# Optimization experiments

Hardware: AMD Instinct MI355X
Metric: run time of the kernel (lower is better)

The kernel has to match this reference:

```python
import jax, jax.numpy as jnp
import numpy as np

N_HEADS = 32
N_KV_HEADS = 8


def _rope_tables(T, half_dim):
    # standard rotary angle tables: theta_i = 10000^(-2i/D)
    inv_freq = 1.0 / (10000.0 ** (np.arange(half_dim, dtype=np.float32) / half_dim))
    ang = np.arange(T, dtype=np.float32)[:, None] * inv_freq[None, :]  # [T, D/2]
    return jnp.asarray(np.sin(ang)), jnp.asarray(np.cos(ang))


def setup_inputs() -> dict:
    key = jax.random.key(0)
    ks = jax.random.split(key, 5)
    B, T, C = 1, 2048, 2048
    hd = C // N_HEADS  # 64
    kv_dim = N_KV_HEADS * hd  # 512
    w_scale = 0.02
    x = jax.random.normal(ks[0], (B, T, C), dtype=jnp.float32)
    Wq = jax.random.normal(ks[1], (C, C), dtype=jnp.float32) * w_scale
    Wk = jax.random.normal(ks[2], (C, kv_dim), dtype=jnp.float32) * w_scale
    Wv = jax.random.normal(ks[3], (C, kv_dim), dtype=jnp.float32) * w_scale
    Wo = jax.random.normal(ks[4], (C, C), dtype=jnp.float32) * w_scale
    rope_sin, rope_cos = _rope_tables(T, hd // 2)
    return {"x": x, "Wq": Wq, "Wk": Wk, "Wv": Wv, "Wo": Wo,
            "rope_sin": rope_sin, "rope_cos": rope_cos, "swa_window": 1024}


def apply_rope(x, sin, cos):
    # x: [B, T, H, D]; sin/cos: [T, D/2]; interleaved-pair rotation
    B, T, H, D = x.shape
    xr = x.reshape(B, T, H, D // 2, 2)
    x1, x2 = xr[..., 0], xr[..., 1]
    s = sin[None, :, None, :]
    c = cos[None, :, None, :]
    o1 = x1 * c - x2 * s
    o2 = x1 * s + x2 * c
    return jnp.stack((o1, o2), axis=-1).reshape(B, T, H, D)


def reference(x, Wq, Wk, Wv, Wo, rope_sin, rope_cos, swa_window):
    B, T, C = x.shape
    hd = C // N_HEADS
    g = N_HEADS // N_KV_HEADS
    q = (x @ Wq).reshape(B, T, N_HEADS, hd)
    k = (x @ Wk).reshape(B, T, N_KV_HEADS, hd)
    v = (x @ Wv).reshape(B, T, N_KV_HEADS, hd)
    q = apply_rope(q, rope_sin, rope_cos)
    k = apply_rope(k, rope_sin, rope_cos)
    # GQA: expand kv heads (repeat_interleave along head dim)
    k = jnp.repeat(k, g, axis=2)
    v = jnp.repeat(v, g, axis=2)
    q = q.transpose(0, 2, 1, 3)  # [B, H, T, D]
    k = k.transpose(0, 2, 1, 3)
    v = v.transpose(0, 2, 1, 3)
    scores = jnp.einsum('bhqd,bhkd->bhqk', q, k) / jnp.sqrt(jnp.float32(hd))
    idx = jnp.arange(T)
    rel = idx[:, None] - idx[None, :]  # query_pos - key_pos
    # masked-out: future tokens (rel < 0) or older than the sliding window
    masked = (rel < 0) | (rel > swa_window)
    scores = jnp.where(masked[None, None], jnp.float32(-1e30), scores)
    attn = jax.nn.softmax(scores, axis=-1)
    out = jnp.einsum('bhqk,bhkd->bhqd', attn, v)
    out = out.transpose(0, 2, 1, 3).reshape(B, T, C)
    return out @ Wo
```

## Files before the change

kernel.cpp:

```cpp
#include <hip/hip_runtime.h>

typedef __attribute__((ext_vector_type(8))) short short8;
typedef __attribute__((ext_vector_type(4))) float f32x4;
typedef unsigned short u16;

#define T_SEQ 2048
#define C_DIM 2048
#define QKV_N 3072
#define HD 64


static __device__ __forceinline__ u16 f2bf(float f) {
    unsigned u = __builtin_bit_cast(unsigned, f);
    unsigned rounding = 0x7fffu + ((u >> 16) & 1u);
    return (u16)((u + rounding) >> 16);
}

static __device__ __forceinline__ void gld_lds16(void* lds, const void* g) {
    __builtin_amdgcn_global_load_lds(
        (const __attribute__((address_space(1))) unsigned int*)g,
        (__attribute__((address_space(3))) unsigned int*)lds, 16, 0, 0);
}


__global__ __launch_bounds__(256) void convert_bf16_k(const float* __restrict__ in,
                                                      u16* __restrict__ out) {
    int i = (blockIdx.x * 256 + threadIdx.x) * 4;
    f32x4 v = *(const f32x4*)(in + i);
    u16* o = out + i;
    o[0] = f2bf(v[0]); o[1] = f2bf(v[1]); o[2] = f2bf(v[2]); o[3] = f2bf(v[3]);
}


__global__ __launch_bounds__(256) void transpose_all(const float* __restrict__ Wq,
                                                     const float* __restrict__ Wk,
                                                     const float* __restrict__ Wv,
                                                     const float* __restrict__ Wo,
                                                     u16* __restrict__ Wt,
                                                     u16* __restrict__ Wot) {
    __shared__ float tile[32][33];
    int bx = blockIdx.x;
    const float* W; u16* D; int N, row_off;
    if (bx < 64)      { W = Wq; D = Wt;  N = 2048; row_off = 0;    }
    else if (bx < 80) { W = Wk; D = Wt;  N = 512;  row_off = 2048; bx -= 64; }
    else if (bx < 96) { W = Wv; D = Wt;  N = 512;  row_off = 2560; bx -= 80; }
    else              { W = Wo; D = Wot; N = 2048; row_off = 0;    bx -= 96; }
    int n0 = bx * 32, k0 = blockIdx.y * 32;
    int tx = threadIdx.x & 31, ty = threadIdx.x >> 5;
#pragma unroll
    for (int i = 0; i < 4; i++)
        tile[ty + i * 8][tx] = W[(size_t)(k0 + ty + i * 8) * N + n0 + tx];
    __syncthreads();
#pragma unroll
    for (int i = 0; i < 4; i++)
        D[(size_t)(row_off + n0 + ty + i * 8) * 2048 + k0 + tx] = f2bf(tile[tx][ty + i * 8]);
}


__global__ __launch_bounds__(256) void gemm_bt(const u16* __restrict__ A,
                                               const u16* __restrict__ BT,
                                               float* __restrict__ C,
                                               int M, int N, int K) {
    __shared__ alignas(16) u16 As[2][128][64];
    __shared__ alignas(16) u16 Bs[2][128][64];
    const int m0 = blockIdx.x * 128;
    const int n0 = blockIdx.y * 128;
    const int w = threadIdx.x >> 6, lane = threadIdx.x & 63;
    const int lo = lane & 15, hi = lane >> 4;
    const int wr = w >> 1, wc = w & 1;
    const int srcsw = ((lane & 7) ^ (lane >> 3)) * 8;

    f32x4 zero4 = {0.f, 0.f, 0.f, 0.f};
    f32x4 acc[4][4];
#pragma unroll
    for (int m = 0; m < 4; m++)
#pragma unroll
        for (int n = 0; n < 4; n++) acc[m][n] = zero4;

    auto stage = [&](int buf, int k0) {
#pragma unroll
        for (int j = 0; j < 4; j++) {
            int row = (w * 4 + j) * 8 + (lane >> 3);
            gld_lds16((char*)&As[buf][0][0] + (w * 4 + j) * 1024,
                      A + (size_t)(m0 + row) * K + k0 + srcsw);
            gld_lds16((char*)&Bs[buf][0][0] + (w * 4 + j) * 1024,
                      BT + (size_t)(n0 + row) * K + k0 + srcsw);
        }
    };

    stage(0, 0);
    __syncthreads();
    const int nk = K >> 6;
    for (int t = 0; t < nk; t++) {
        const int cur = t & 1;
        if (t + 1 < nk) stage(cur ^ 1, (t + 1) * 64);
#pragma unroll
        for (int kk = 0; kk < 2; kk++) {
            short8 a[4], b[4];
#pragma unroll
            for (int m = 0; m < 4; m++) {
                int r = wr * 64 + m * 16 + lo;
                a[m] = *(const short8*)((const char*)&As[cur][0][0] + r * 128 + (((kk * 4 + hi) ^ (lo & 7)) << 4));
            }
#pragma unroll
            for (int n = 0; n < 4; n++) {
                int r = wc * 64 + n * 16 + lo;
                b[n] = *(const short8*)((const char*)&Bs[cur][0][0] + r * 128 + (((kk * 4 + hi) ^ (lo & 7)) << 4));
            }
#pragma unroll
            for (int m = 0; m < 4; m++)
#pragma unroll
                for (int n = 0; n < 4; n++)
                    acc[m][n] = __builtin_amdgcn_mfma_f32_16x16x32_bf16(a[m], b[n], acc[m][n], 0, 0, 0);
        }
        __syncthreads();
    }
#pragma unroll
    for (int m = 0; m < 4; m++)
#pragma unroll
        for (int n = 0; n < 4; n++) {
            int col = n0 + wc * 64 + n * 16 + lo;
#pragma unroll
            for (int r = 0; r < 4; r++) {
                int row = m0 + wr * 64 + m * 16 + hi * 4 + r;
                C[(size_t)row * N + col] = acc[m][n][r];
            }
        }
}


__global__ __launch_bounds__(256) void rope_conv(const float* __restrict__ qkv,
                                                 const float* __restrict__ sn,
                                                 const float* __restrict__ cs,
                                                 u16* __restrict__ qb,
                                                 u16* __restrict__ kb,
                                                 u16* __restrict__ vt) {
    int t = blockIdx.x / 6;
    int idx = (blockIdx.x % 6) * 256 + threadIdx.x;
    const float* row = qkv + (size_t)t * QKV_N;
    if (idx < 1024) {
        int h = idx >> 5, pr = idx & 31;
        float x1 = row[h * 64 + 2 * pr], x2 = row[h * 64 + 2 * pr + 1];
        float s = sn[t * 32 + pr], c = cs[t * 32 + pr];
        float o1 = (x1 * c - x2 * s) * 0.125f;
        float o2 = (x1 * s + x2 * c) * 0.125f;
        unsigned pack = (unsigned)f2bf(o1) | ((unsigned)f2bf(o2) << 16);
        *(unsigned*)(qb + (size_t)t * C_DIM + h * 64 + 2 * pr) = pack;
    } else if (idx < 1280) {
        int j = idx - 1024;
        int kh = j >> 5, pr = j & 31;
        float x1 = row[2048 + kh * 64 + 2 * pr], x2 = row[2048 + kh * 64 + 2 * pr + 1];
        float s = sn[t * 32 + pr], c = cs[t * 32 + pr];
        float o1 = x1 * c - x2 * s;
        float o2 = x1 * s + x2 * c;
        unsigned pack = (unsigned)f2bf(o1) | ((unsigned)f2bf(o2) << 16);
        *(unsigned*)(kb + ((size_t)kh * T_SEQ + t) * 64 + 2 * pr) = pack;
    } else {
        int j = idx - 1280;
        int kh = j >> 5, dl = (j & 31) * 2;
        float v0 = row[2560 + kh * 64 + dl], v1 = row[2560 + kh * 64 + dl + 1];
        vt[((size_t)kh * 64 + dl) * T_SEQ + t] = f2bf(v0);
        vt[((size_t)kh * 64 + dl + 1) * T_SEQ + t] = f2bf(v1);
    }
}


__global__ __launch_bounds__(256) void attn_fwd(const u16* __restrict__ qb,
                                                const u16* __restrict__ kb,
                                                const u16* __restrict__ vt,
                                                u16* __restrict__ ob,
                                                const int* __restrict__ winp) {
    __shared__ alignas(16) char KsB[2][8192];
    __shared__ alignas(16) char VsB[2][8192];
    __shared__ alignas(16) u16 Ps[4][16][88];
    const int window = *winp;
    const int h = blockIdx.y, kvh = h >> 2;
    const int q0 = blockIdx.x * 64;
    const int w = threadIdx.x >> 6, lane = threadIdx.x & 63;
    const int lo = lane & 15, hi = lane >> 4;

    const int qrow = q0 + w * 16 + lo;
    const short8 qa0 = *(const short8*)(qb + (size_t)qrow * C_DIM + h * HD + hi * 8);
    const short8 qa1 = *(const short8*)(qb + (size_t)qrow * C_DIM + h * HD + 32 + hi * 8);

    f32x4 zero4 = {0.f, 0.f, 0.f, 0.f};
    f32x4 acc[4];
#pragma unroll
    for (int dt = 0; dt < 4; dt++) acc[dt] = zero4;
    float lreg[4] = {0.f, 0.f, 0.f, 0.f};

    int kt0 = q0 - window; if (kt0 < 0) kt0 = 0; kt0 &= ~63;
    const int qlo_w = q0 + w * 16, qhi_w = qlo_w + 15;
    const int nt = (q0 + 64 - kt0) >> 6;

    auto stage = [&](int buf, int kt) {
#pragma unroll
        for (int j = 0; j < 2; j++) {
            int c = (w * 2 + j) * 64 + lane;
            int rr = c >> 3, sc = (c & 7) ^ (rr & 7);
            gld_lds16(KsB[buf] + (w * 2 + j) * 1024,
                      kb + ((size_t)kvh * T_SEQ + kt + rr) * 64 + sc * 8);
            gld_lds16(VsB[buf] + (w * 2 + j) * 1024,
                      vt + ((size_t)kvh * 64 + rr) * T_SEQ + kt + sc * 8);
        }
    };

    stage(0, kt0);
    __syncthreads();
    for (int i = 0; i < nt; i++) {
        const int kt = kt0 + i * 64;
        const int cur = i & 1;
        if (i + 1 < nt) stage(cur ^ 1, kt + 64);
        if (kt <= qhi_w && kt + 63 >= qlo_w - window) {
            const bool interior = (kt + 63 <= qlo_w) && (qhi_w - kt <= window);
            f32x4 s0, s1, s2, s3;
            {
#define QK_TILE(SD, NT)                                                              \
                {                                                                    \
                    int key = (NT) * 16 + lo;                                        \
                    const short8 kf0 = *(const short8*)(KsB[cur] + key * 128 + ((hi ^ (key & 7)) << 4));       \
                    const short8 kf1 = *(const short8*)(KsB[cur] + key * 128 + (((4 + hi) ^ (key & 7)) << 4)); \
                    f32x4 z = zero4;                                                 \
                    z = __builtin_amdgcn_mfma_f32_16x16x32_bf16(qa0, kf0, z, 0, 0, 0);\
                    z = __builtin_amdgcn_mfma_f32_16x16x32_bf16(qa1, kf1, z, 0, 0, 0);\
                    SD = z;                                                          \
                }
                QK_TILE(s0, 0) QK_TILE(s1, 1) QK_TILE(s2, 2) QK_TILE(s3, 3)
#undef QK_TILE
            }
            if (!interior) {
#define MASK_TILE(SD, NT)                                                            \
                {                                                                    \
                    int key = kt + (NT) * 16 + lo;                                   \
                    _Pragma("unroll")                                                \
                    for (int r = 0; r < 4; r++) {                                    \
                        int q = qlo_w + hi * 4 + r;                                  \
                        if ((unsigned)(q - key) > (unsigned)window) SD[r] = -1e30f;  \
                    }                                                                \
                }
                MASK_TILE(s0, 0) MASK_TILE(s1, 1) MASK_TILE(s2, 2) MASK_TILE(s3, 3)
#undef MASK_TILE
            }
#define EXP_TILE(SD, NT)                                                             \
            {                                                                        \
                _Pragma("unroll")                                                    \
                for (int r = 0; r < 4; r++) {                                        \
                    float p = __expf(SD[r]);                                         \
                    lreg[r] += p;                                                    \
                    Ps[w][hi * 4 + r][(NT) * 16 + lo] = f2bf(p);                     \
                }                                                                    \
            }
            EXP_TILE(s0, 0) EXP_TILE(s1, 1) EXP_TILE(s2, 2) EXP_TILE(s3, 3)
#undef EXP_TILE
            const short8 pa0 = *(const short8*)&Ps[w][lo][hi * 8];
            const short8 pa1 = *(const short8*)&Ps[w][lo][32 + hi * 8];
#pragma unroll
            for (int dt = 0; dt < 4; dt++) {
                int d = dt * 16 + lo;
                const short8 vf0 = *(const short8*)(VsB[cur] + d * 128 + ((hi ^ (d & 7)) << 4));
                const short8 vf1 = *(const short8*)(VsB[cur] + d * 128 + (((4 + hi) ^ (d & 7)) << 4));
                acc[dt] = __builtin_amdgcn_mfma_f32_16x16x32_bf16(pa0, vf0, acc[dt], 0, 0, 0);
                acc[dt] = __builtin_amdgcn_mfma_f32_16x16x32_bf16(pa1, vf1, acc[dt], 0, 0, 0);
            }
        }
        __syncthreads();
    }
    float inv[4];
#pragma unroll
    for (int r = 0; r < 4; r++) {
        float l = lreg[r];
        l += __shfl_xor(l, 1);
        l += __shfl_xor(l, 2);
        l += __shfl_xor(l, 4);
        l += __shfl_xor(l, 8);
        inv[r] = 1.0f / l;
    }
#pragma unroll
    for (int dt = 0; dt < 4; dt++)
#pragma unroll
        for (int r = 0; r < 4; r++) {
            int q = qlo_w + hi * 4 + r;
            ob[(size_t)q * C_DIM + h * HD + dt * 16 + lo] = f2bf(acc[dt][r] * inv[r]);
        }
}


extern "C" void kernel_launch(void* const* d_in, const int* in_sizes, int n_in,
                              void* d_out, int out_size, void* d_ws, size_t ws_size,
                              hipStream_t stream) {
    const float* x  = (const float*)d_in[0];
    const float* Wq = (const float*)d_in[1];
    const float* Wk = (const float*)d_in[2];
    const float* Wv = (const float*)d_in[3];
    const float* Wo = (const float*)d_in[4];
    const float* rs = (const float*)d_in[5];
    const float* rc = (const float*)d_in[6];
    const int*  win = (const int*)d_in[7];
    float* out = (float*)d_out;

    char* w = (char*)d_ws;
    u16*   xb   = (u16*)(w);
    u16*   Wt   = (u16*)(w + (8ull  << 20));
    u16*   Wot  = (u16*)(w + (20ull << 20));
    float* qkv  = (float*)(w + (28ull << 20));
    u16*   qb   = (u16*)(w + (52ull << 20));
    u16*   kbuf = (u16*)(w + (60ull << 20));
    u16*   vtb  = (u16*)(w + (62ull << 20));
    u16*   attb = (u16*)(w + (64ull << 20));

    convert_bf16_k<<<4096, 256, 0, stream>>>(x, xb);
    transpose_all<<<dim3(160, 64), 256, 0, stream>>>(Wq, Wk, Wv, Wo, Wt, Wot);
    gemm_bt<<<dim3(16, 24), 256, 0, stream>>>(xb, Wt, qkv, 2048, 3072, 2048);
    rope_conv<<<2048 * 6, 256, 0, stream>>>(qkv, rs, rc, qb, kbuf, vtb);
    attn_fwd<<<dim3(32, 32), 256, 0, stream>>>(qb, kbuf, vtb, attb, win);
    gemm_bt<<<dim3(16, 16), 256, 0, stream>>>(attb, Wot, out, 2048, 2048, 2048);
}
```

Baseline: 248.4 us.

## Template GEMM N-tile width for more blocks; swizzle P tile and add setprio

Makes the GEMM N-tile width a template parameter (96 columns for the QKV projection, 64 for the output projection). Both launches then use 512 blocks instead of 384 and 256, giving better occupancy and wave balance across the CUs. In attention, the padded P scratch tile is replaced by an XOR-swizzled unpadded layout to avoid LDS bank conflicts while using less LDS. s_setprio is raised around the MFMA sections. Narrower N tiles lower the reuse of the A tile and add global traffic.

```diff
diff --git a/kernel.cpp b/kernel.cpp
--- a/kernel.cpp
+++ b/kernel.cpp
@@ -57,34 +57,42 @@
 }
 
 
+template <int NF>
 __global__ __launch_bounds__(256) void gemm_bt(const u16* __restrict__ A,
                                                const u16* __restrict__ BT,
                                                float* __restrict__ C,
                                                int M, int N, int K) {
     __shared__ alignas(16) u16 As[2][128][64];
-    __shared__ alignas(16) u16 Bs[2][128][64];
+    __shared__ alignas(16) u16 Bs[2][32 * NF][64];
     const int m0 = blockIdx.x * 128;
-    const int n0 = blockIdx.y * 128;
+    const int bn0 = blockIdx.y * (32 * NF);
     const int w = threadIdx.x >> 6, lane = threadIdx.x & 63;
     const int lo = lane & 15, hi = lane >> 4;
     const int wr = w >> 1, wc = w & 1;
     const int srcsw = ((lane & 7) ^ (lane >> 3)) * 8;
 
     f32x4 zero4 = {0.f, 0.f, 0.f, 0.f};
-    f32x4 acc[4][4];
+    f32x4 acc[4][NF];
 #pragma unroll
     for (int m = 0; m < 4; m++)
 #pragma unroll
-        for (int n = 0; n < 4; n++) acc[m][n] = zero4;
-
+        for (int n = 0; n < NF; n++) acc[m][n] = zero4;
+
+    const int NSEG = 16 + 4 * NF;
     auto stage = [&](int buf, int k0) {
 #pragma unroll
-        for (int j = 0; j < 4; j++) {
-            int row = (w * 4 + j) * 8 + (lane >> 3);
-            gld_lds16((char*)&As[buf][0][0] + (w * 4 + j) * 1024,
-                      A + (size_t)(m0 + row) * K + k0 + srcsw);
-            gld_lds16((char*)&Bs[buf][0][0] + (w * 4 + j) * 1024,
-                      BT + (size_t)(n0 + row) * K + k0 + srcsw);
+        for (int j = 0; j < NSEG / 4; j++) {
+            int s = j * 4 + w;
+            if (s < 16) {
+                int row = s * 8 + (lane >> 3);
+                gld_lds16((char*)&As[buf][0][0] + s * 1024,
+                          A + (size_t)(m0 + row) * K + k0 + srcsw);
+            } else {
+                int s2 = s - 16;
+                int row = s2 * 8 + (lane >> 3);
+                gld_lds16((char*)&Bs[buf][0][0] + s2 * 1024,
+                          BT + (size_t)(bn0 + row) * K + k0 + srcsw);
+            }
         }
     };
 
@@ -96,21 +104,22 @@
         if (t + 1 < nk) stage(cur ^ 1, (t + 1) * 64);
 #pragma unroll
         for (int kk = 0; kk < 2; kk++) {
-            short8 a[4], b[4];
+            const int csw = ((kk * 4 + hi) ^ (lo & 7)) << 4;
+            short8 a[4], b[NF];
 #pragma unroll
             for (int m = 0; m < 4; m++) {
                 int r = wr * 64 + m * 16 + lo;
-                a[m] = *(const short8*)((const char*)&As[cur][0][0] + r * 128 + (((kk * 4 + hi) ^ (lo & 7)) << 4));
-            }
-#pragma unroll
-            for (int n = 0; n < 4; n++) {
-                int r = wc * 64 + n * 16 + lo;
-                b[n] = *(const short8*)((const char*)&Bs[cur][0][0] + r * 128 + (((kk * 4 + hi) ^ (lo & 7)) << 4));
+                a[m] = *(const short8*)((const char*)&As[cur][0][0] + r * 128 + csw);
+            }
+#pragma unroll
+            for (int n = 0; n < NF; n++) {
+                int r = wc * 16 * NF + n * 16 + lo;
+                b[n] = *(const short8*)((const char*)&Bs[cur][0][0] + r * 128 + csw);
             }
 #pragma unroll
             for (int m = 0; m < 4; m++)
 #pragma unroll
-                for (int n = 0; n < 4; n++)
+                for (int n = 0; n < NF; n++)
                     acc[m][n] = __builtin_amdgcn_mfma_f32_16x16x32_bf16(a[m], b[n], acc[m][n], 0, 0, 0);
         }
         __syncthreads();
@@ -118,8 +127,8 @@
 #pragma unroll
     for (int m = 0; m < 4; m++)
 #pragma unroll
-        for (int n = 0; n < 4; n++) {
-            int col = n0 + wc * 64 + n * 16 + lo;
+        for (int n = 0; n < NF; n++) {
+            int col = bn0 + wc * 16 * NF + n * 16 + lo;
 #pragma unroll
             for (int r = 0; r < 4; r++) {
                 int row = m0 + wr * 64 + m * 16 + hi * 4 + r;
@@ -172,7 +181,7 @@
                                                 const int* __restrict__ winp) {
     __shared__ alignas(16) char KsB[2][8192];
     __shared__ alignas(16) char VsB[2][8192];
-    __shared__ alignas(16) u16 Ps[4][16][88];
+    __shared__ alignas(16) u16 Ps[4][16][64];
     const int window = *winp;
     const int h = blockIdx.y, kvh = h >> 2;
     const int q0 = blockIdx.x * 64;
@@ -214,6 +223,7 @@
         if (kt <= qhi_w && kt + 63 >= qlo_w - window) {
             const bool interior = (kt + 63 <= qlo_w) && (qhi_w - kt <= window);
             f32x4 s0, s1, s2, s3;
+            __builtin_amdgcn_s_setprio(1);
             {
 #define QK_TILE(SD, NT)                                                              \
                 {                                                                    \
@@ -228,6 +238,7 @@
                 QK_TILE(s0, 0) QK_TILE(s1, 1) QK_TILE(s2, 2) QK_TILE(s3, 3)
 #undef QK_TILE
             }
+            __builtin_amdgcn_s_setprio(0);
             if (!interior) {
 #define MASK_TILE(SD, NT)                                                            \
                 {                                                                    \
@@ -247,13 +258,15 @@
                 for (int r = 0; r < 4; r++) {                                        \
                     float p = __expf(SD[r]);                                         \
                     lreg[r] += p;                                                    \
-                    Ps[w][hi * 4 + r][(NT) * 16 + lo] = f2bf(p);                     \
+                    int q16 = hi * 4 + r;                                            \
+                    Ps[w][q16][((NT) * 16 + lo) ^ ((q16 & 7) << 3)] = f2bf(p);       \
                 }                                                                    \
             }
             EXP_TILE(s0, 0) EXP_TILE(s1, 1) EXP_TILE(s2, 2) EXP_TILE(s3, 3)
 #undef EXP_TILE
-            const short8 pa0 = *(const short8*)&Ps[w][lo][hi * 8];
-            const short8 pa1 = *(const short8*)&Ps[w][lo][32 + hi * 8];
+            const short8 pa0 = *(const short8*)&Ps[w][lo][(hi ^ (lo & 7)) << 3];
+            const short8 pa1 = *(const short8*)&Ps[w][lo][((4 + hi) ^ (lo & 7)) << 3];
+            __builtin_amdgcn_s_setprio(1);
 #pragma unroll
             for (int dt = 0; dt < 4; dt++) {
                 int d = dt * 16 + lo;
@@ -262,6 +275,7 @@
                 acc[dt] = __builtin_amdgcn_mfma_f32_16x16x32_bf16(pa0, vf0, acc[dt], 0, 0, 0);
                 acc[dt] = __builtin_amdgcn_mfma_f32_16x16x32_bf16(pa1, vf1, acc[dt], 0, 0, 0);
             }
+            __builtin_amdgcn_s_setprio(0);
         }
         __syncthreads();
     }
@@ -310,8 +324,8 @@
 
     convert_bf16_k<<<4096, 256, 0, stream>>>(x, xb);
     transpose_all<<<dim3(160, 64), 256, 0, stream>>>(Wq, Wk, Wv, Wo, Wt, Wot);
-    gemm_bt<<<dim3(16, 24), 256, 0, stream>>>(xb, Wt, qkv, 2048, 3072, 2048);
+    gemm_bt<3><<<dim3(16, 32), 256, 0, stream>>>(xb, Wt, qkv, 2048, 3072, 2048);
     rope_conv<<<2048 * 6, 256, 0, stream>>>(qkv, rs, rc, qb, kbuf, vtb);
     attn_fwd<<<dim3(32, 32), 256, 0, stream>>>(qb, kbuf, vtb, attb, win);
-    gemm_bt<<<dim3(16, 16), 256, 0, stream>>>(attb, Wot, out, 2048, 2048, 2048);
-}
+    gemm_bt<2><<<dim3(16, 32), 256, 0, stream>>>(attb, Wot, out, 2048, 2048, 2048);
+}
```

New measurement: 228.6 us. 8.0% less time.
